# Performance work log

Hardware: AMD Instinct MI355X
Metric: run time of the kernel (lower is better)

The kernel has to match this reference:

```python
import jax, jax.numpy as jnp
import numpy as np

B, S, D = 2, 2048, 1024
H = 16
DK = D // H
FF = 4096
EPS = 1e-6


def setup_inputs() -> dict:
    key = jax.random.key(0)
    ks = jax.random.split(key, 16)
    sd = 0.02
    inp = {
        "x": jax.random.normal(ks[0], (B, S, D), dtype=jnp.float32),
        # attention projections (stored as [in, out]; y = x @ W + b)
        "Wq": jax.random.normal(ks[1], (D, D), dtype=jnp.float32) * sd,
        "bq": jnp.zeros((D,), jnp.float32),
        "Wk": jax.random.normal(ks[2], (D, D), dtype=jnp.float32) * sd,
        "bk": jnp.zeros((D,), jnp.float32),
        "Wv": jax.random.normal(ks[3], (D, D), dtype=jnp.float32) * sd,
        "bv": jnp.zeros((D,), jnp.float32),
        "Wo": jax.random.normal(ks[4], (D, D), dtype=jnp.float32) * sd,
        "bo": jnp.zeros((D,), jnp.float32),
        # FFN
        "W1": jax.random.normal(ks[5], (D, FF), dtype=jnp.float32) * sd,
        "b1": jnp.zeros((FF,), jnp.float32),
        "W2": jax.random.normal(ks[6], (FF, D), dtype=jnp.float32) * sd,
        "b2": jnp.zeros((D,), jnp.float32),
        # LayerNorms (pre-norm)
        "ln1_g": jnp.ones((D,), jnp.float32),
        "ln1_b": jnp.zeros((D,), jnp.float32),
        "ln2_g": jnp.ones((D,), jnp.float32),
        "ln2_b": jnp.zeros((D,), jnp.float32),
    }
    return inp


def _layer_norm(x, g, b):
    mu = jnp.mean(x, axis=-1, keepdims=True)
    var = jnp.mean(jnp.square(x - mu), axis=-1, keepdims=True)
    return (x - mu) * jax.lax.rsqrt(var + EPS) * g + b


def _attention(x, Wq, bq, Wk, bk, Wv, bv, Wo, bo):
    # project and split heads: [B,S,D] -> [B,H,S,DK]
    def split(t):
        return t.reshape(B, S, H, DK).transpose(0, 2, 1, 3)
    q = split(x @ Wq + bq)
    k = split(x @ Wk + bk)
    v = split(x @ Wv + bv)
    scores = jnp.einsum("bhqd,bhkd->bhqk", q, k) / jnp.sqrt(jnp.float32(DK))
    p = jax.nn.softmax(scores, axis=-1)  # no mask in forward path; dropout eval-mode
    o = jnp.einsum("bhqk,bhkd->bhqd", p, v)
    o = o.transpose(0, 2, 1, 3).reshape(B, S, D)
    return o @ Wo + bo


def reference(x, Wq, bq, Wk, bk, Wv, bv, Wo, bo, W1, b1, W2, b2,
              ln1_g, ln1_b, ln2_g, ln2_b):
    # sublayer 1: x + attn(LN(x))
    x = x + _attention(_layer_norm(x, ln1_g, ln1_b), Wq, bq, Wk, bk, Wv, bv, Wo, bo)
    # sublayer 2: x + FFN(LN(x))
    h = jax.nn.relu(_layer_norm(x, ln2_g, ln2_b) @ W1 + b1)
    x = x + (h @ W2 + b2)
    return x
```

## Files before the change

kernel.cpp:

```cpp
#include <hip/hip_runtime.h>


#define S_LEN 2048
#define DMODEL 1024
#define NHEADS 16
#define FFDIM 4096
#define MROWS 4096

typedef _Float16 f16;
typedef _Float16 f16x8 __attribute__((ext_vector_type(8)));
typedef __fp16 fp16x2 __attribute__((ext_vector_type(2)));
typedef float f32x4 __attribute__((ext_vector_type(4)));
typedef unsigned int u32;
typedef unsigned long long u64;
typedef unsigned long long u64x2 __attribute__((ext_vector_type(2)));

union Frag { f16x8 h; u64 q[2]; f16 e[8]; u32 w[4]; };

__device__ __forceinline__ f32x4 mfma16(f16x8 a, f16x8 b, f32x4 c) {
  return __builtin_amdgcn_mfma_f32_16x16x32_f16(a, b, c, 0, 0, 0);
}

__device__ __forceinline__ u32 pk16(float lo, float hi) {
  fp16x2 v = __builtin_amdgcn_cvt_pkrtz(lo, hi);
  return __builtin_bit_cast(u32, v);
}

typedef __attribute__((address_space(1))) const void gvoid;
typedef __attribute__((address_space(3))) void lvoid;

__device__ __forceinline__ void gload16(const f16* gp, f16* lp) {
  __builtin_amdgcn_global_load_lds((gvoid*)gp, (lvoid*)lp, 16, 0, 0);
}

__global__ __launch_bounds__(256) void wtrans4_kernel(const float* __restrict__ W0,
                                                      const float* __restrict__ W1,
                                                      const float* __restrict__ W2,
                                                      const float* __restrict__ W3,
                                                      f16* __restrict__ D0,
                                                      f16* __restrict__ D1,
                                                      f16* __restrict__ D2,
                                                      f16* __restrict__ D3) {
  const int z = blockIdx.z;
  const float* W = z == 0 ? W0 : z == 1 ? W1 : z == 2 ? W2 : W3;
  f16* Wt = z == 0 ? D0 : z == 1 ? D1 : z == 2 ? D2 : D3;
  __shared__ f16 tile[32][33];
  const int n0 = blockIdx.x * 32, k0 = blockIdx.y * 32;
  const int tx = threadIdx.x & 31, ty = threadIdx.x >> 5;
  for (int i = 0; i < 4; i++) {
    int k = ty + i * 8;
    tile[k][tx] = (f16)W[(size_t)(k0 + k) * 1024 + n0 + tx];
  }
  __syncthreads();
  for (int i = 0; i < 4; i++) {
    int n = ty + i * 8;
    Wt[(size_t)(n0 + n) * 1024 + k0 + tx] = tile[tx][n];
  }
}

__global__ __launch_bounds__(256) void wtrans2_kernel(const float* __restrict__ W1,
                                                      const float* __restrict__ W2,
                                                      f16* __restrict__ D1,
                                                      f16* __restrict__ D2) {
  const int z = blockIdx.z;
  const float* W = z ? W2 : W1;
  f16* Wt = z ? D2 : D1;
  const int K = z ? 4096 : 1024, N = z ? 1024 : 4096;
  const int n0 = (z ? blockIdx.y : blockIdx.x) * 32;
  const int k0 = (z ? blockIdx.x : blockIdx.y) * 32;
  __shared__ f16 tile[32][33];
  const int tx = threadIdx.x & 31, ty = threadIdx.x >> 5;
  for (int i = 0; i < 4; i++) {
    int k = ty + i * 8;
    tile[k][tx] = (f16)W[(size_t)(k0 + k) * N + n0 + tx];
  }
  __syncthreads();
  for (int i = 0; i < 4; i++) {
    int n = ty + i * 8;
    Wt[(size_t)(n0 + n) * K + k0 + tx] = tile[tx][n];
  }
}

__global__ void bias_concat_kernel(const float* __restrict__ bq,
                                   const float* __restrict__ bk,
                                   const float* __restrict__ bv,
                                   float* __restrict__ out) {
  int i = blockIdx.x * 256 + threadIdx.x;
  float v = (i < 1024) ? bq[i] : (i < 2048) ? bk[i - 1024] : bv[i - 2048];
  out[i] = v;
}

__global__ __launch_bounds__(256) void ln_kernel(const float* __restrict__ x,
                                                 const float* __restrict__ gw,
                                                 const float* __restrict__ bw,
                                                 f16* __restrict__ out) {
  const int row = blockIdx.x, t = threadIdx.x;
  const float* xr = x + (size_t)row * DMODEL;
  float4 v = *(const float4*)(xr + t * 4);
  float s = v.x + v.y + v.z + v.w;
  float s2 = v.x * v.x + v.y * v.y + v.z * v.z + v.w * v.w;
  for (int off = 1; off < 64; off <<= 1) {
    s += __shfl_xor(s, off);
    s2 += __shfl_xor(s2, off);
  }
  __shared__ float red[8];
  const int w = t >> 6, lane = t & 63;
  if (lane == 0) { red[w] = s; red[w + 4] = s2; }
  __syncthreads();
  s = red[0] + red[1] + red[2] + red[3];
  s2 = red[4] + red[5] + red[6] + red[7];
  float mu = s * (1.0f / DMODEL);
  float var = s2 * (1.0f / DMODEL) - mu * mu;
  float rstd = rsqrtf(var + 1e-6f);
  float4 g4 = *(const float4*)(gw + t * 4);
  float4 b4 = *(const float4*)(bw + t * 4);
  union { f16 h[4]; u64 q; } o;
  o.h[0] = (f16)((v.x - mu) * rstd * g4.x + b4.x);
  o.h[1] = (f16)((v.y - mu) * rstd * g4.y + b4.y);
  o.h[2] = (f16)((v.z - mu) * rstd * g4.z + b4.z);
  o.h[3] = (f16)((v.w - mu) * rstd * g4.w + b4.w);
  *(u64*)(out + (size_t)row * DMODEL + t * 4) = o.q;
}

__global__ __launch_bounds__(512, 2) void gemm8(const f16* __restrict__ A, int lda,
                                                const f16* __restrict__ Bt, int ldb,
                                                const float* __restrict__ bias,
                                                f16* __restrict__ outh, int ldo,
                                                int K, int relu) {
  __shared__ f16 As[2][256 * 64];
  __shared__ f16 Bs[2][256 * 64];
  const int gx = gridDim.x;
  const int nwg = gx * gridDim.y;
  int id = blockIdx.y * gx + blockIdx.x;
  id = (id & 7) * (nwg >> 3) + (id >> 3);
  const int m0 = (id / gx) * 256, n0 = (id % gx) * 256;
  const int t = threadIdx.x;
  const int lane = t & 63, w = t >> 6;
  const int wr = w >> 2, wc = w & 3;
  const int rA = lane & 15, g = lane >> 4;

  f32x4 acc[8][4] = {};

  auto stageA = [&](int ts, int buf) {
    const int k0 = ts * 64;
#pragma unroll
    for (int p = 0; p < 4; p++) {
      const int chunk = p * 512 + t;
      const int row = chunk >> 3;
      const int cbg = ((chunk & 7) ^ (row & 7)) * 8;
      gload16(A + (size_t)(m0 + row) * lda + k0 + cbg,
              &As[buf][(p * 512 + w * 64) * 8]);
    }
  };
  auto stageB = [&](int ts, int buf) {
    const int k0 = ts * 64;
#pragma unroll
    for (int p = 0; p < 4; p++) {
      const int chunk = p * 512 + t;
      const int row = chunk >> 3;
      const int cbg = ((chunk & 7) ^ (row & 7)) * 8;
      gload16(Bt + (size_t)(n0 + row) * ldb + k0 + cbg,
              &Bs[buf][(p * 512 + w * 64) * 8]);
    }
  };

  auto compute = [&](int cur) {
#pragma unroll
    for (int ks = 0; ks < 2; ks++) {
      Frag b[4];
#pragma unroll
      for (int nt = 0; nt < 4; nt++) {
        const int row = wc * 64 + nt * 16 + rA;
        b[nt].h = *(const f16x8*)(&Bs[cur][row * 64 + ((ks * 4 + g) ^ (row & 7)) * 8]);
      }
#pragma unroll
      for (int mt = 0; mt < 8; mt++) {
        const int row = wr * 128 + mt * 16 + rA;
        Frag a;
        a.h = *(const f16x8*)(&As[cur][row * 64 + ((ks * 4 + g) ^ (row & 7)) * 8]);
#pragma unroll
        for (int nt = 0; nt < 4; nt++)
          acc[mt][nt] = mfma16(a.h, b[nt].h, acc[mt][nt]);
      }
    }
  };

  const int nt_steps = K / 64;
  stageA(0, 0); stageB(0, 0);
  stageA(1, 1); stageB(1, 1);

  for (int ts = 0; ts < nt_steps; ++ts) {
    const int cur = ts & 1;
    if (ts + 1 < nt_steps)
      asm volatile("s_waitcnt vmcnt(8)" ::: "memory");
    else
      asm volatile("s_waitcnt vmcnt(0)" ::: "memory");
    __builtin_amdgcn_sched_barrier(0);
    __builtin_amdgcn_s_barrier();
    compute(cur);
    asm volatile("s_waitcnt lgkmcnt(0)" ::: "memory");
    __builtin_amdgcn_sched_barrier(0);
    __builtin_amdgcn_s_barrier();
    if (ts + 2 < nt_steps) { stageA(ts + 2, cur); stageB(ts + 2, cur); }
  }

#pragma unroll
  for (int mt = 0; mt < 8; mt++) {
#pragma unroll
    for (int nt = 0; nt < 4; nt++) {
      const int col = n0 + wc * 64 + nt * 16 + rA;
      const int rowb = m0 + wr * 128 + mt * 16 + g * 4;
      const float bs = bias[col];
#pragma unroll
      for (int r = 0; r < 4; r++) {
        float v = acc[mt][nt][r] + bs;
        if (relu) v = fmaxf(v, 0.0f);
        outh[(size_t)(rowb + r) * ldo + col] = (f16)v;
      }
    }
  }
}

template <int BM, int BN>
__global__ __launch_bounds__(256, 2) void gemm2(const f16* __restrict__ A, int lda,
                                                const f16* __restrict__ Bt, int ldb,
                                                const float* __restrict__ bias,
                                                const float* __restrict__ res,
                                                float* __restrict__ outf,
                                                f16* __restrict__ outh, int ldo,
                                                int N, int K, int relu) {
  constexpr int MT = BM / 32, NT = BN / 32;
  constexpr int NLOADS = BM / 32 + BN / 32;
  __shared__ f16 As[2][BM * 64];
  __shared__ f16 Bs[2][BN * 64];
  const int gx = gridDim.x;
  const int nwg = gx * gridDim.y;
  int id = blockIdx.y * gx + blockIdx.x;
  id = (id & 7) * (nwg >> 3) + (id >> 3);
  const int m0 = (id / gx) * BM, n0 = (id % gx) * BN;
  const int t = threadIdx.x;
  const int lane = t & 63, w = t >> 6;
  const int wr = w >> 1, wc = w & 1;
  const int rA = lane & 15, g = lane >> 4;

  f32x4 acc[MT][NT] = {};

  auto stage = [&](int ts, int buf) {
    const int k0 = ts * 64;
#pragma unroll
    for (int p = 0; p < BM / 32; p++) {
      const int chunk = p * 256 + w * 64 + lane;
      const int row = chunk >> 3;
      const int cbg = ((chunk & 7) ^ (row & 7)) * 8;
      gload16(A + (size_t)(m0 + row) * lda + k0 + cbg,
              &As[buf][(p * 256 + w * 64) * 8]);
    }
#pragma unroll
    for (int p = 0; p < BN / 32; p++) {
      const int chunk = p * 256 + w * 64 + lane;
      const int row = chunk >> 3;
      const int cbg = ((chunk & 7) ^ (row & 7)) * 8;
      gload16(Bt + (size_t)(n0 + row) * ldb + k0 + cbg,
              &Bs[buf][(p * 256 + w * 64) * 8]);
    }
  };

  auto compute = [&](int cur) {
#pragma unroll
    for (int ks = 0; ks < 2; ks++) {
      Frag a[MT], b[NT];
#pragma unroll
      for (int mt = 0; mt < MT; mt++) {
        const int row = wr * (BM / 2) + mt * 16 + rA;
        a[mt].h = *(const f16x8*)(&As[cur][row * 64 + ((ks * 4 + g) ^ (row & 7)) * 8]);
      }
#pragma unroll
      for (int nt = 0; nt < NT; nt++) {
        const int row = wc * (BN / 2) + nt * 16 + rA;
        b[nt].h = *(const f16x8*)(&Bs[cur][row * 64 + ((ks * 4 + g) ^ (row & 7)) * 8]);
      }
#pragma unroll
      for (int mt = 0; mt < MT; mt++)
#pragma unroll
        for (int nt = 0; nt < NT; nt++)
          acc[mt][nt] = mfma16(a[mt].h, b[nt].h, acc[mt][nt]);
    }
  };

  const int nsteps = K / 64;
  stage(0, 0);
  stage(1, 1);

  for (int ts = 0; ts < nsteps; ++ts) {
    const int cur = ts & 1;
    if (ts + 1 < nsteps)
      asm volatile("s_waitcnt vmcnt(%0)" :: "i"(NLOADS) : "memory");
    else
      asm volatile("s_waitcnt vmcnt(0)" ::: "memory");
    __builtin_amdgcn_sched_barrier(0);
    __builtin_amdgcn_s_barrier();
    compute(cur);
    asm volatile("s_waitcnt lgkmcnt(0)" ::: "memory");
    __builtin_amdgcn_sched_barrier(0);
    __builtin_amdgcn_s_barrier();
    if (ts + 2 < nsteps) stage(ts + 2, cur);
  }

#pragma unroll
  for (int mt = 0; mt < MT; mt++) {
#pragma unroll
    for (int nt = 0; nt < NT; nt++) {
      const int col = n0 + wc * (BN / 2) + nt * 16 + rA;
      const int rowb = m0 + wr * (BM / 2) + mt * 16 + g * 4;
      const float bs = bias[col];
#pragma unroll
      for (int r = 0; r < 4; r++) {
        float v = acc[mt][nt][r] + bs;
        if (relu) v = fmaxf(v, 0.0f);
        if (res) v += res[(size_t)(rowb + r) * N + col];
        if (outf) outf[(size_t)(rowb + r) * N + col] = v;
        if (outh) outh[(size_t)(rowb + r) * ldo + col] = (f16)v;
      }
    }
  }
}

__global__ __launch_bounds__(256) void vtrans_kernel(const f16* __restrict__ qkv,
                                                     f16* __restrict__ vt) {
  const int bh = blockIdx.y;
  const int s0 = blockIdx.x * 64;
  const int b = bh >> 4, h = bh & 15;
  __shared__ f16 tile[64][72];
  const int t = threadIdx.x;
  for (int pass = 0; pass < 2; pass++) {
    int sl = (t >> 3) + pass * 32;
    int dk0 = (t & 7) * 8;
    u64x2 v = *(const u64x2*)(qkv + (size_t)(b * S_LEN + s0 + sl) * 3072 + 2048 + h * 64 + dk0);
    *(u64x2*)(&tile[sl][dk0]) = v;
  }
  __syncthreads();
  for (int pass = 0; pass < 2; pass++) {
    int dk = (t >> 3) + pass * 32;
    int sc = (t & 7) * 8;
    union { u64x2 q; f16 u[8]; } o;
    for (int j = 0; j < 8; j++) {
      int pos = sc + j;
      int kv = (pos & 32) | ((pos & 4) << 2) | ((pos & 0x18) >> 1) | (pos & 3);
      o.u[j] = tile[kv][dk];
    }
    *(u64x2*)(vt + (size_t)(bh * 64 + dk) * S_LEN + s0 + sc) = o.q;
  }
}

__global__ __launch_bounds__(256, 2) void attn_kernel(const f16* __restrict__ qkv,
                                                      const f16* __restrict__ vt,
                                                      f16* __restrict__ attn_out) {
  const int s_id = blockIdx.x;
  const int bh = (s_id & 7) * 4 + ((s_id >> 3) & 3);
  const int qt0 = (s_id >> 5) * 128;
  const int b = bh >> 4, h = bh & 15;
  const int t = threadIdx.x;
  const int lane = t & 63, w = t >> 6;
  const int rA = lane & 15, g = lane >> 4;

  __shared__ f16 Ks[2][64 * 64];
  __shared__ f16 Vs[2][64 * 64];

  Frag qf[2][2];
#pragma unroll
  for (int qg = 0; qg < 2; qg++)
#pragma unroll
    for (int kt = 0; kt < 2; kt++) {
      const f16* p = qkv + (size_t)(b * S_LEN + qt0 + w * 32 + qg * 16 + rA) * 3072 +
                     h * 64 + kt * 32 + 8 * g;
      f16x8 v = *(const f16x8*)p;
#pragma unroll
      for (int j = 0; j < 8; j++) v[j] = v[j] * (f16)0.18033688f;
      qf[qg][kt].h = v;
    }

  float lRp[2] = {0.0f, 0.0f};
  f32x4 o2[2][4] = {};

#define STAGE_KV(kv0_, buf_)                                                     \
  {                                                                              \
    _Pragma("unroll") for (int i = 0; i < 2; i++) {                              \
      int C = i * 256 + w * 64 + lane;                                           \
      int row = C >> 3;                                                          \
      int cbg = ((C & 7) ^ (row & 7)) * 8;                                       \
      gload16(qkv + (size_t)(b * S_LEN + (kv0_) + row) * 3072 + 1024 + h * 64 + cbg, \
              &Ks[buf_][(i * 256 + w * 64) * 8]);                                \
      gload16(vt + (size_t)(bh * 64 + row) * S_LEN + (kv0_) + cbg,               \
              &Vs[buf_][(i * 256 + w * 64) * 8]);                                \
    }                                                                            \
  }

  int cur = 0;
  STAGE_KV(0, 0);

  for (int kv0 = 0; kv0 < S_LEN; kv0 += 64) {
    __syncthreads();
    if (kv0 + 64 < S_LEN) STAGE_KV(kv0 + 64, cur ^ 1);

    Frag kf[4][2];
#pragma unroll
    for (int nt = 0; nt < 4; nt++)
#pragma unroll
      for (int kt = 0; kt < 2; kt++) {
        const int row = nt * 16 + rA;
        kf[nt][kt].h = *(const f16x8*)(&Ks[cur][row * 64 + ((kt * 4 + g) ^ (row & 7)) * 8]);
      }
    f32x4 s[2][4] = {};
#pragma unroll
    for (int qg = 0; qg < 2; qg++)
#pragma unroll
      for (int nt = 0; nt < 4; nt++)
#pragma unroll
        for (int kt = 0; kt < 2; kt++)
          s[qg][nt] = mfma16(kf[nt][kt].h, qf[qg][kt].h, s[qg][nt]);

    Frag ph[2][2];
#pragma unroll
    for (int qg = 0; qg < 2; qg++) {
      float rs = 0.0f;
#pragma unroll
      for (int nt = 0; nt < 4; nt++)
#pragma unroll
        for (int r = 0; r < 4; r++) {
          float e0 = exp2f(s[qg][nt][r]);
          s[qg][nt][r] = e0;
          rs += e0;
        }
      lRp[qg] += rs;
#pragma unroll
      for (int j = 0; j < 2; j++) {
        ph[qg][j].w[0] = pk16(s[qg][2 * j][0], s[qg][2 * j][1]);
        ph[qg][j].w[1] = pk16(s[qg][2 * j][2], s[qg][2 * j][3]);
        ph[qg][j].w[2] = pk16(s[qg][2 * j + 1][0], s[qg][2 * j + 1][1]);
        ph[qg][j].w[3] = pk16(s[qg][2 * j + 1][2], s[qg][2 * j + 1][3]);
      }
    }

#pragma unroll
    for (int ntd = 0; ntd < 4; ntd++) {
      const int row = ntd * 16 + rA;
#pragma unroll
      for (int j = 0; j < 2; j++) {
        Frag vf;
        vf.h = *(const f16x8*)(&Vs[cur][row * 64 + ((j * 4 + g) ^ (row & 7)) * 8]);
#pragma unroll
        for (int qg = 0; qg < 2; qg++)
          o2[qg][ntd] = mfma16(vf.h, ph[qg][j].h, o2[qg][ntd]);
      }
    }

    cur ^= 1;
  }

#pragma unroll
  for (int qg = 0; qg < 2; qg++) {
    float l = lRp[qg];
    l += __shfl_xor(l, 16);
    l += __shfl_xor(l, 32);
    const float inv = 1.0f / l;
    const int qrow = qt0 + w * 32 + qg * 16 + rA;
#pragma unroll
    for (int ntd = 0; ntd < 4; ntd++) {
      union { f16 h[4]; u64 q; } pk;
#pragma unroll
      for (int r = 0; r < 4; r++) pk.h[r] = (f16)(o2[qg][ntd][r] * inv);
      *(u64*)(attn_out + (size_t)(b * S_LEN + qrow) * DMODEL + h * 64 + ntd * 16 + g * 4) = pk.q;
    }
  }
#undef STAGE_KV
}

extern "C" void kernel_launch(void* const* d_in, const int* in_sizes, int n_in,
                              void* d_out, int out_size, void* d_ws, size_t ws_size,
                              hipStream_t stream) {
  const float* x     = (const float*)d_in[0];
  const float* Wq    = (const float*)d_in[1];
  const float* bq    = (const float*)d_in[2];
  const float* Wk    = (const float*)d_in[3];
  const float* bk    = (const float*)d_in[4];
  const float* Wv    = (const float*)d_in[5];
  const float* bv    = (const float*)d_in[6];
  const float* Wo    = (const float*)d_in[7];
  const float* bo    = (const float*)d_in[8];
  const float* W1    = (const float*)d_in[9];
  const float* b1    = (const float*)d_in[10];
  const float* W2    = (const float*)d_in[11];
  const float* b2    = (const float*)d_in[12];
  const float* ln1g  = (const float*)d_in[13];
  const float* ln1b  = (const float*)d_in[14];
  const float* ln2g  = (const float*)d_in[15];
  const float* ln2b  = (const float*)d_in[16];
  float* out = (float*)d_out;
  char* ws = (char*)d_ws;

  size_t off = 0;
  f16* wqkv_t = (f16*)(ws + off); off += (size_t)3072 * 1024 * 2;
  f16* wo_t   = (f16*)(ws + off); off += (size_t)1024 * 1024 * 2;
  f16* w1_t   = (f16*)(ws + off); off += (size_t)4096 * 1024 * 2;
  f16* w2_t   = (f16*)(ws + off); off += (size_t)1024 * 4096 * 2;
  float* bqkv = (float*)(ws + off); off += 3072 * 4;
  f16* regB   = (f16*)(ws + off); off += (size_t)MROWS * 1024 * 2;
  f16* qkv    = (f16*)(ws + off); off += (size_t)MROWS * 3072 * 2;
  f16* vt     = (f16*)(ws + off); off += (size_t)MROWS * 1024 * 2;
  f16* hbuf   = qkv;

  wtrans4_kernel<<<dim3(32, 32, 4), 256, 0, stream>>>(
      Wq, Wk, Wv, Wo,
      wqkv_t, wqkv_t + (size_t)1024 * 1024, wqkv_t + (size_t)2048 * 1024, wo_t);
  wtrans2_kernel<<<dim3(128, 32, 2), 256, 0, stream>>>(W1, W2, w1_t, w2_t);
  bias_concat_kernel<<<12, 256, 0, stream>>>(bq, bk, bv, bqkv);

  ln_kernel<<<MROWS, 256, 0, stream>>>(x, ln1g, ln1b, regB);

  gemm8<<<dim3(12, 16), 512, 0, stream>>>(regB, 1024, wqkv_t, 1024, bqkv,
                                          qkv, 3072, 1024, 0);
  vtrans_kernel<<<dim3(32, 32), 256, 0, stream>>>(qkv, vt);

  attn_kernel<<<512, 256, 0, stream>>>(qkv, vt, regB);

  gemm2<128, 64><<<dim3(16, 32), 256, 0, stream>>>(regB, 1024, wo_t, 1024, bo,
                                                   x, out, nullptr, 0,
                                                   1024, 1024, 0);
  ln_kernel<<<MROWS, 256, 0, stream>>>(out, ln2g, ln2b, regB);

  gemm8<<<dim3(16, 16), 512, 0, stream>>>(regB, 1024, w1_t, 1024, b1,
                                          hbuf, 4096, 1024, 1);
  gemm2<128, 64><<<dim3(16, 32), 256, 0, stream>>>(hbuf, 4096, w2_t, 4096, b2,
                                                   out, out, nullptr, 0,
                                                   1024, 4096, 0);
}
```

Before: 254.1 us.

## Fuse V transpose into QKV GEMM epilogue and merge weight-transpose launches

```diff
diff --git a/kernel.cpp b/kernel.cpp
--- a/kernel.cpp
+++ b/kernel.cpp
@@ -33,41 +33,33 @@
   __builtin_amdgcn_global_load_lds((gvoid*)gp, (lvoid*)lp, 16, 0, 0);
 }
 
-__global__ __launch_bounds__(256) void wtrans4_kernel(const float* __restrict__ W0,
+__global__ __launch_bounds__(256) void wtrans6_kernel(const float* __restrict__ Wq,
+                                                      const float* __restrict__ Wk,
+                                                      const float* __restrict__ Wv,
+                                                      const float* __restrict__ Wo,
                                                       const float* __restrict__ W1,
                                                       const float* __restrict__ W2,
-                                                      const float* __restrict__ W3,
-                                                      f16* __restrict__ D0,
-                                                      f16* __restrict__ D1,
-                                                      f16* __restrict__ D2,
-                                                      f16* __restrict__ D3) {
-  const int z = blockIdx.z;
-  const float* W = z == 0 ? W0 : z == 1 ? W1 : z == 2 ? W2 : W3;
-  f16* Wt = z == 0 ? D0 : z == 1 ? D1 : z == 2 ? D2 : D3;
-  __shared__ f16 tile[32][33];
-  const int n0 = blockIdx.x * 32, k0 = blockIdx.y * 32;
-  const int tx = threadIdx.x & 31, ty = threadIdx.x >> 5;
-  for (int i = 0; i < 4; i++) {
-    int k = ty + i * 8;
-    tile[k][tx] = (f16)W[(size_t)(k0 + k) * 1024 + n0 + tx];
-  }
-  __syncthreads();
-  for (int i = 0; i < 4; i++) {
-    int n = ty + i * 8;
-    Wt[(size_t)(n0 + n) * 1024 + k0 + tx] = tile[tx][n];
-  }
-}
-
-__global__ __launch_bounds__(256) void wtrans2_kernel(const float* __restrict__ W1,
-                                                      const float* __restrict__ W2,
+                                                      f16* __restrict__ Dqkv,
+                                                      f16* __restrict__ Do,
                                                       f16* __restrict__ D1,
                                                       f16* __restrict__ D2) {
   const int z = blockIdx.z;
-  const float* W = z ? W2 : W1;
-  f16* Wt = z ? D2 : D1;
-  const int K = z ? 4096 : 1024, N = z ? 1024 : 4096;
-  const int n0 = (z ? blockIdx.y : blockIdx.x) * 32;
-  const int k0 = (z ? blockIdx.x : blockIdx.y) * 32;
+  const float* W;
+  f16* Wt;
+  int K, N, n0, k0;
+  if (z < 4) {
+    if (blockIdx.x >= 32) return;
+    W = z == 0 ? Wq : z == 1 ? Wk : z == 2 ? Wv : Wo;
+    Wt = z == 3 ? Do : Dqkv + (size_t)z * 1024 * 1024;
+    K = 1024; N = 1024;
+    n0 = blockIdx.x * 32; k0 = blockIdx.y * 32;
+  } else if (z == 4) {
+    W = W1; Wt = D1; K = 1024; N = 4096;
+    n0 = blockIdx.x * 32; k0 = blockIdx.y * 32;
+  } else {
+    W = W2; Wt = D2; K = 4096; N = 1024;
+    n0 = blockIdx.y * 32; k0 = blockIdx.x * 32;
+  }
   __shared__ f16 tile[32][33];
   const int tx = threadIdx.x & 31, ty = threadIdx.x >> 5;
   for (int i = 0; i < 4; i++) {
@@ -126,6 +118,7 @@
                                                 const f16* __restrict__ Bt, int ldb,
                                                 const float* __restrict__ bias,
                                                 f16* __restrict__ outh, int ldo,
+                                                f16* __restrict__ vt,
                                                 int K, int relu) {
   __shared__ f16 As[2][256 * 64];
   __shared__ f16 Bs[2][256 * 64];
@@ -211,11 +204,24 @@
       const int col = n0 + wc * 64 + nt * 16 + rA;
       const int rowb = m0 + wr * 128 + mt * 16 + g * 4;
       const float bs = bias[col];
-#pragma unroll
-      for (int r = 0; r < 4; r++) {
-        float v = acc[mt][nt][r] + bs;
-        if (relu) v = fmaxf(v, 0.0f);
-        outh[(size_t)(rowb + r) * ldo + col] = (f16)v;
+      const bool isv = (vt != nullptr) && (col >= 2048);
+      if (isv) {
+        const int h = (col - 2048) >> 6, dk = (col - 2048) & 63;
+        const int b = rowb >> 11;
+        const int sl = rowb & 2047;
+        const int low = sl & 63;
+        const int posb = (low & 32) | ((low & 16) >> 2) | ((low & 8) << 1) | ((low & 4) << 1);
+        union { f16 h4[4]; u64 q; } pk;
+#pragma unroll
+        for (int r = 0; r < 4; r++) pk.h4[r] = (f16)(acc[mt][nt][r] + bs);
+        *(u64*)(vt + (size_t)((b * 16 + h) * 64 + dk) * S_LEN + (sl & ~63) + posb) = pk.q;
+      } else {
+#pragma unroll
+        for (int r = 0; r < 4; r++) {
+          float v = acc[mt][nt][r] + bs;
+          if (relu) v = fmaxf(v, 0.0f);
+          outh[(size_t)(rowb + r) * ldo + col] = (f16)v;
+        }
       }
     }
   }
@@ -322,33 +328,6 @@
         if (outh) outh[(size_t)(rowb + r) * ldo + col] = (f16)v;
       }
     }
-  }
-}
-
-__global__ __launch_bounds__(256) void vtrans_kernel(const f16* __restrict__ qkv,
-                                                     f16* __restrict__ vt) {
-  const int bh = blockIdx.y;
-  const int s0 = blockIdx.x * 64;
-  const int b = bh >> 4, h = bh & 15;
-  __shared__ f16 tile[64][72];
-  const int t = threadIdx.x;
-  for (int pass = 0; pass < 2; pass++) {
-    int sl = (t >> 3) + pass * 32;
-    int dk0 = (t & 7) * 8;
-    u64x2 v = *(const u64x2*)(qkv + (size_t)(b * S_LEN + s0 + sl) * 3072 + 2048 + h * 64 + dk0);
-    *(u64x2*)(&tile[sl][dk0]) = v;
-  }
-  __syncthreads();
-  for (int pass = 0; pass < 2; pass++) {
-    int dk = (t >> 3) + pass * 32;
-    int sc = (t & 7) * 8;
-    union { u64x2 q; f16 u[8]; } o;
-    for (int j = 0; j < 8; j++) {
-      int pos = sc + j;
-      int kv = (pos & 32) | ((pos & 4) << 2) | ((pos & 0x18) >> 1) | (pos & 3);
-      o.u[j] = tile[kv][dk];
-    }
-    *(u64x2*)(vt + (size_t)(bh * 64 + dk) * S_LEN + s0 + sc) = o.q;
   }
 }
 
@@ -509,17 +488,14 @@
   f16* vt     = (f16*)(ws + off); off += (size_t)MROWS * 1024 * 2;
   f16* hbuf   = qkv;
 
-  wtrans4_kernel<<<dim3(32, 32, 4), 256, 0, stream>>>(
-      Wq, Wk, Wv, Wo,
-      wqkv_t, wqkv_t + (size_t)1024 * 1024, wqkv_t + (size_t)2048 * 1024, wo_t);
-  wtrans2_kernel<<<dim3(128, 32, 2), 256, 0, stream>>>(W1, W2, w1_t, w2_t);
+  wtrans6_kernel<<<dim3(128, 32, 6), 256, 0, stream>>>(
+      Wq, Wk, Wv, Wo, W1, W2, wqkv_t, wo_t, w1_t, w2_t);
   bias_concat_kernel<<<12, 256, 0, stream>>>(bq, bk, bv, bqkv);
 
   ln_kernel<<<MROWS, 256, 0, stream>>>(x, ln1g, ln1b, regB);
 
   gemm8<<<dim3(12, 16), 512, 0, stream>>>(regB, 1024, wqkv_t, 1024, bqkv,
-                                          qkv, 3072, 1024, 0);
-  vtrans_kernel<<<dim3(32, 32), 256, 0, stream>>>(qkv, vt);
+                                          qkv, 3072, vt, 1024, 0);
 
   attn_kernel<<<512, 256, 0, stream>>>(qkv, vt, regB);
 
@@ -529,7 +505,7 @@
   ln_kernel<<<MROWS, 256, 0, stream>>>(out, ln2g, ln2b, regB);
 
   gemm8<<<dim3(16, 16), 512, 0, stream>>>(regB, 1024, w1_t, 1024, b1,
-                                          hbuf, 4096, 1024, 1);
+                                          hbuf, 4096, nullptr, 1024, 1);
   gemm2<128, 64><<<dim3(16, 32), 256, 0, stream>>>(hbuf, 4096, w2_t, 4096, b2,
                                                    out, out, nullptr, 0,
                                                    1024, 4096, 0);
```

Result: no change. 254.0 us (-0.1%).
